# Kernel optimization log

Measured on AMD Instinct MI355X. Metric: run time of the kernel, lower is better.

Reference implementation:

```python
import jax, jax.numpy as jnp
import numpy as np

N = 50000          # nodes
E = 800000         # edges (before self loops)
IN_C = 128
HEADS = 4
D = 64             # out_per_head
HID = HEADS * D    # 256
OUT_C = 128
NEG_SLOPE = 0.2


def setup_inputs() -> dict:
    key = jax.random.key(0)
    ks = jax.random.split(key, 20)
    x = jax.random.normal(ks[0], (N, IN_C), dtype=jnp.float32)
    edge_index = jax.random.randint(ks[1], (2, E), 0, N, dtype=jnp.int32)
    s = 0.05
    params = {}
    dims = [IN_C, HID, HID]
    for i in range(3):
        params[f"W{i+1}"] = jax.random.normal(ks[2 + 4 * i], (dims[i], HID), dtype=jnp.float32) * s
        params[f"a_src{i+1}"] = jax.random.normal(ks[3 + 4 * i], (HEADS, D), dtype=jnp.float32) * s
        params[f"a_dst{i+1}"] = jax.random.normal(ks[4 + 4 * i], (HEADS, D), dtype=jnp.float32) * s
        params[f"b{i+1}"] = jnp.zeros((HID,), dtype=jnp.float32)
    params["head_W"] = jax.random.normal(ks[14], (HID, OUT_C), dtype=jnp.float32) * s
    params["head_b"] = jnp.zeros((OUT_C,), dtype=jnp.float32)
    return {"x": x, "edge_index": edge_index, **params}


def _gat_layer(x, src, dst, W, a_src, a_dst, b):
    # project: [N, heads, D]
    h = (x @ W).reshape(-1, HEADS, D)
    # per-node attention halves: [N, heads]
    alpha_s = jnp.einsum("nhd,hd->nh", h, a_src)
    alpha_d = jnp.einsum("nhd,hd->nh", h, a_dst)
    # per-edge logits: [E, heads]
    logits = jax.nn.leaky_relu(alpha_s[src] + alpha_d[dst], negative_slope=NEG_SLOPE)
    # segment softmax over incoming edges of each dst node
    seg_max = jax.ops.segment_max(logits, dst, num_segments=N)
    e = jnp.exp(logits - seg_max[dst])
    seg_sum = jax.ops.segment_sum(e, dst, num_segments=N)
    alpha = e / (seg_sum[dst] + 1e-16)
    # weighted messages, scatter-aggregate: [N, heads, D]
    msg = h[src] * alpha[:, :, None]
    out = jax.ops.segment_sum(msg, dst, num_segments=N)
    return out.reshape(-1, HID) + b


def reference(x, edge_index, W1, a_src1, a_dst1, b1, W2, a_src2, a_dst2, b2,
              W3, a_src3, a_dst3, b3, head_W, head_b):
    # add self loops once (add_self_loops=True in every GATConv)
    loop = jnp.arange(N, dtype=edge_index.dtype)
    src = jnp.concatenate([edge_index[0], loop])
    dst = jnp.concatenate([edge_index[1], loop])
    h = x
    layers = [(W1, a_src1, a_dst1, b1), (W2, a_src2, a_dst2, b2), (W3, a_src3, a_dst3, b3)]
    for (W, a_s, a_d, b) in layers:
        h = jax.nn.elu(_gat_layer(h, src, dst, W, a_s, a_d, b))
        # dropout inactive in eval mode
    graph_emb = jnp.mean(h, axis=0)          # global_mean_pool over single graph
    logits = graph_emb @ head_W + head_b     # [OUT_C]
    return logits
```

## Files before the change

kernel.cpp:

```cpp
#include <hip/hip_runtime.h>
#include <stdint.h>

#define NN 50000
#define EE 800000
#define ET 850000
#define INC 128
#define HID 256
#define OUTC 128
#define NB ((NN + 255) / 256)

typedef __attribute__((ext_vector_type(4))) float f32x4;
typedef __attribute__((ext_vector_type(8))) short s16x8;
typedef __attribute__((ext_vector_type(4))) short s16x4;

static __device__ __forceinline__ float b2f(unsigned short u){
  union { float f; unsigned int i; } v; v.i = ((unsigned int)u) << 16; return v.f;
}
static __device__ __forceinline__ unsigned short f2b(float f){
  union { float f; unsigned int i; } v; v.f = f;
  unsigned int r = v.i + 0x7FFFu + ((v.i >> 16) & 1u);
  return (unsigned short)(r >> 16);
}

__global__ void k_degree(const int* __restrict__ ei, int* __restrict__ cnt){
  int e = blockIdx.x * 256 + threadIdx.x;
  if (e >= ET) return;
  int d = (e < EE) ? ei[EE + e] : (e - EE);
  atomicAdd(&cnt[d], 1);
}

__global__ void k_blockscan(int* __restrict__ cnt, int* __restrict__ off,
                            int* __restrict__ bsum){
  __shared__ int s[256];
  int b = blockIdx.x, tid = threadIdx.x;
  int i = b * 256 + tid;
  int v = (i < NN) ? cnt[i] : 0;
  if (i < NN) cnt[i] = 0;
  s[tid] = v; __syncthreads();
  #pragma unroll
  for (int o = 1; o < 256; o <<= 1){
    int t = (tid >= o) ? s[tid - o] : 0; __syncthreads();
    s[tid] += t; __syncthreads();
  }
  if (i < NN) off[i] = s[tid] - v;
  if (tid == 255) bsum[b] = s[255];
}

__global__ void k_scanb(const int* __restrict__ bsum, int* __restrict__ bbase){
  __shared__ int s[256];
  int tid = threadIdx.x;
  int v = (tid < NB) ? bsum[tid] : 0;
  s[tid] = v; __syncthreads();
  #pragma unroll
  for (int o = 1; o < 256; o <<= 1){
    int t = (tid >= o) ? s[tid - o] : 0; __syncthreads();
    s[tid] += t; __syncthreads();
  }
  if (tid < NB) bbase[tid] = s[tid] - v;
}

__global__ void k_addback(int* __restrict__ off, const int* __restrict__ bbase){
  int b = blockIdx.x, tid = threadIdx.x;
  int i = b * 256 + tid;
  if (i < NN) off[i] += bbase[b];
  if (i == 0) off[NN] = ET;
}

__global__ void k_scatter(const int* __restrict__ ei, const int* __restrict__ off,
                          int* __restrict__ cnt, int* __restrict__ ssrc){
  int e = blockIdx.x * 256 + threadIdx.x;
  if (e >= ET) return;
  int s, d;
  if (e < EE){ s = ei[e]; d = ei[EE + e]; } else { s = e - EE; d = s; }
  int p = off[d] + atomicAdd(&cnt[d], 1);
  ssrc[p] = s;
}

__global__ void k_transposeAll(const float* __restrict__ W1, const float* __restrict__ W2,
                               const float* __restrict__ W3, unsigned short* __restrict__ T1,
                               unsigned short* __restrict__ T2, unsigned short* __restrict__ T3){
  int b = blockIdx.x;
  const float* W; unsigned short* WT; int K, base;
  if (b < 128)      { W = W1; WT = T1; K = 128; base = 0; }
  else if (b < 384) { W = W2; WT = T2; K = 256; base = 128; }
  else              { W = W3; WT = T3; K = 256; base = 384; }
  int idx = (b - base) * 256 + threadIdx.x;
  int k = idx >> 8, c = idx & 255;
  WT[c * K + k] = f2b(W[idx]);
}

template<bool AF32>
__global__ __launch_bounds__(256) void k_gemm_fused(const void* __restrict__ Av,
    const unsigned short* __restrict__ WT,
    const float* __restrict__ a_src, const float* __restrict__ a_dst,
    unsigned short* __restrict__ C, float* __restrict__ as_, float* __restrict__ ad_,
    int M, int K){
  __shared__ unsigned short sMem[64 * 258];
  unsigned short (*sA)[64][72]  = (unsigned short (*)[64][72])sMem;
  unsigned short (*sC)[258] = (unsigned short (*)[258])sMem;
  int tid = threadIdx.x;
  int wave = tid >> 6, lane = tid & 63;
  int bm0 = blockIdx.x * 64;
  int wc0 = wave * 64;
  f32x4 acc[4][4];
  #pragma unroll
  for (int i = 0; i < 4; i++)
    #pragma unroll
    for (int j = 0; j < 4; j++) acc[i][j] = (f32x4){0.f, 0.f, 0.f, 0.f};

  s16x8 regs[2];
  int li0 = tid, li1 = tid + 256;
  int r0 = li0 >> 3, kb0 = (li0 & 7) * 8;
  int r1 = li1 >> 3, kb1 = (li1 & 7) * 8;

  auto ldA = [&](int k0){
    #pragma unroll
    for (int i = 0; i < 2; i++){
      int rr = i ? r1 : r0, kb = i ? kb1 : kb0;
      int gr = bm0 + rr;
      if constexpr (AF32){
        const float* A = (const float*)Av;
        unsigned short t[8] = {0,0,0,0,0,0,0,0};
        if (gr < M){
          const float4* p = (const float4*)(A + (size_t)gr * K + k0 + kb);
          float4 v0 = p[0], v1 = p[1];
          t[0]=f2b(v0.x); t[1]=f2b(v0.y); t[2]=f2b(v0.z); t[3]=f2b(v0.w);
          t[4]=f2b(v1.x); t[5]=f2b(v1.y); t[6]=f2b(v1.z); t[7]=f2b(v1.w);
        }
        regs[i] = *(s16x8*)t;
      } else {
        const unsigned short* A = (const unsigned short*)Av;
        s16x8 v = (s16x8){0,0,0,0,0,0,0,0};
        if (gr < M) v = *(const s16x8*)(A + (size_t)gr * K + k0 + kb);
        regs[i] = v;
      }
    }
  };
  auto stA = [&](int buf){
    *(s16x8*)&sA[buf][r0][kb0] = regs[0];
    *(s16x8*)&sA[buf][r1][kb1] = regs[1];
  };

  int T = K >> 6;
  ldA(0); stA(0);
  __syncthreads();
  for (int t = 0; t < T; t++){
    int k0 = t << 6;
    if (t + 1 < T) ldA(k0 + 64);
    int cur = t & 1;
    #pragma unroll
    for (int kk = 0; kk < 64; kk += 32){
      int kl = kk + (lane >> 4) * 8;
      s16x8 af[4], bf[4];
      #pragma unroll
      for (int ni = 0; ni < 4; ni++)
        bf[ni] = *(const s16x8*)(WT + (size_t)(wc0 + ni * 16 + (lane & 15)) * K + k0 + kl);
      #pragma unroll
      for (int mi = 0; mi < 4; mi++) af[mi] = *(const s16x8*)&sA[cur][mi * 16 + (lane & 15)][kl];
      #pragma unroll
      for (int mi = 0; mi < 4; mi++)
        #pragma unroll
        for (int ni = 0; ni < 4; ni++)
          acc[mi][ni] = __builtin_amdgcn_mfma_f32_16x16x32_bf16(af[mi], bf[ni], acc[mi][ni], 0, 0, 0);
    }
    if (t + 1 < T) stA(cur ^ 1);
    __syncthreads();
  }

  #pragma unroll
  for (int mi = 0; mi < 4; mi++){
    #pragma unroll
    for (int ni = 0; ni < 4; ni++){
      int col = wc0 + ni * 16 + (lane & 15);
      int rb = mi * 16 + (lane >> 4) * 4;
      #pragma unroll
      for (int r = 0; r < 4; r++){
        int row = rb + r;
        unsigned short us = f2b(acc[mi][ni][r]);
        sC[row][col] = us;
        if (bm0 + row < M) C[(size_t)(bm0 + row) * HID + col] = us;
      }
    }
  }
  __syncthreads();
  {
    int q = wave, r = lane;
    float ps = 0.f, pd = 0.f;
    #pragma unroll 8
    for (int d = 0; d < 64; d++){
      float hv = b2f(sC[r][q * 64 + d]);
      ps += hv * a_src[q * 64 + d];
      pd += hv * a_dst[q * 64 + d];
    }
    if (bm0 + r < M){
      as_[(size_t)(bm0 + r) * 4 + q] = ps;
      ad_[(size_t)(bm0 + r) * 4 + q] = pd;
    }
  }
}

__global__ __launch_bounds__(256) void k_aggregate(const int* __restrict__ off,
    const int* __restrict__ ssrc, const float* __restrict__ as_, const float* __restrict__ ad_,
    const unsigned short* __restrict__ h, const float* __restrict__ bias,
    unsigned short* __restrict__ out){
  int gid = blockIdx.x * 256 + threadIdx.x;
  int wid = gid >> 6, lane = gid & 63;
  if (wid >= NN) return;
  int start = off[wid], end = off[wid + 1], e1 = end - 1;
  int hq = lane >> 4;
  float ad2 = ad_[(size_t)wid * 4 + hq];
  float sA_ = 0.f, sB_ = 0.f;
  f32x4 A = {0,0,0,0}, B = {0,0,0,0}, Cc = {0,0,0,0}, D = {0,0,0,0};

  int p = start;
  int j0 = ssrc[p];
  int j1 = ssrc[min(p + 1, e1)], j2 = ssrc[min(p + 2, e1)], j3 = ssrc[min(p + 3, e1)];
  int j4 = ssrc[min(p + 4, e1)], j5 = ssrc[min(p + 5, e1)];
  int j6 = ssrc[min(p + 6, e1)], j7 = ssrc[min(p + 7, e1)];
  s16x4 r0 = *(const s16x4*)(h + (size_t)j0 * HID + lane * 4);
  s16x4 r1 = *(const s16x4*)(h + (size_t)j1 * HID + lane * 4);
  s16x4 r2 = *(const s16x4*)(h + (size_t)j2 * HID + lane * 4);
  s16x4 r3 = *(const s16x4*)(h + (size_t)j3 * HID + lane * 4);
  float a0 = as_[(size_t)j0 * 4 + hq], a1 = as_[(size_t)j1 * 4 + hq];
  float a2 = as_[(size_t)j2 * 4 + hq], a3 = as_[(size_t)j3 * 4 + hq];

  for (; p + 3 < end; p += 4){
    s16x4 u0 = *(const s16x4*)(h + (size_t)j4 * HID + lane * 4);
    s16x4 u1 = *(const s16x4*)(h + (size_t)j5 * HID + lane * 4);
    s16x4 u2 = *(const s16x4*)(h + (size_t)j6 * HID + lane * 4);
    s16x4 u3 = *(const s16x4*)(h + (size_t)j7 * HID + lane * 4);
    float b0 = as_[(size_t)j4 * 4 + hq], b1 = as_[(size_t)j5 * 4 + hq];
    float b2 = as_[(size_t)j6 * 4 + hq], b3 = as_[(size_t)j7 * 4 + hq];
    int t0 = ssrc[min(p + 8, e1)],  t1 = ssrc[min(p + 9, e1)];
    int t2 = ssrc[min(p + 10, e1)], t3 = ssrc[min(p + 11, e1)];
    float l0 = a0 + ad2; l0 = l0 > 0.f ? l0 : 0.2f * l0;
    float l1 = a1 + ad2; l1 = l1 > 0.f ? l1 : 0.2f * l1;
    float l2 = a2 + ad2; l2 = l2 > 0.f ? l2 : 0.2f * l2;
    float l3 = a3 + ad2; l3 = l3 > 0.f ? l3 : 0.2f * l3;
    float w0 = __expf(fminf(l0, 60.f)), w1 = __expf(fminf(l1, 60.f));
    float w2 = __expf(fminf(l2, 60.f)), w3 = __expf(fminf(l3, 60.f));
    sA_ += w0 + w2; sB_ += w1 + w3;
    #pragma unroll
    for (int c = 0; c < 4; c++){
      A[c]  += w0 * b2f((unsigned short)r0[c]);
      B[c]  += w1 * b2f((unsigned short)r1[c]);
      Cc[c] += w2 * b2f((unsigned short)r2[c]);
      D[c]  += w3 * b2f((unsigned short)r3[c]);
    }
    j0 = j4; j1 = j5; j2 = j6; j3 = j7;
    j4 = t0; j5 = t1; j6 = t2; j7 = t3;
    r0 = u0; r1 = u1; r2 = u2; r3 = u3;
    a0 = b0; a1 = b1; a2 = b2; a3 = b3;
  }
  int rem = end - p;
  if (rem > 0){
    float l = a0 + ad2; l = l > 0.f ? l : 0.2f * l;
    float w = __expf(fminf(l, 60.f)); sA_ += w;
    #pragma unroll
    for (int c = 0; c < 4; c++) A[c]  += w * b2f((unsigned short)r0[c]);
  }
  if (rem > 1){
    float l = a1 + ad2; l = l > 0.f ? l : 0.2f * l;
    float w = __expf(fminf(l, 60.f)); sB_ += w;
    #pragma unroll
    for (int c = 0; c < 4; c++) B[c]  += w * b2f((unsigned short)r1[c]);
  }
  if (rem > 2){
    float l = a2 + ad2; l = l > 0.f ? l : 0.2f * l;
    float w = __expf(fminf(l, 60.f)); sA_ += w;
    #pragma unroll
    for (int c = 0; c < 4; c++) Cc[c] += w * b2f((unsigned short)r2[c]);
  }

  float inv = 1.f / (sA_ + sB_ + 1e-16f);
  float4 bv = *(const float4*)(bias + lane * 4);
  float o0 = (A[0] + B[0] + Cc[0] + D[0]) * inv + bv.x;
  float o1 = (A[1] + B[1] + Cc[1] + D[1]) * inv + bv.y;
  float o2 = (A[2] + B[2] + Cc[2] + D[2]) * inv + bv.z;
  float o3 = (A[3] + B[3] + Cc[3] + D[3]) * inv + bv.w;
  o0 = o0 > 0.f ? o0 : (__expf(o0) - 1.f);
  o1 = o1 > 0.f ? o1 : (__expf(o1) - 1.f);
  o2 = o2 > 0.f ? o2 : (__expf(o2) - 1.f);
  o3 = o3 > 0.f ? o3 : (__expf(o3) - 1.f);
  s16x4 ov;
  ov[0] = (short)f2b(o0); ov[1] = (short)f2b(o1);
  ov[2] = (short)f2b(o2); ov[3] = (short)f2b(o3);
  *(s16x4*)(out + (size_t)wid * HID + lane * 4) = ov;
}

__global__ __launch_bounds__(256) void k_pool(const unsigned short* __restrict__ X,
                                              float* __restrict__ pool){
  int b = blockIdx.x, c = threadIdx.x;
  int n0 = b * 64, n1 = min(n0 + 64, NN);
  float acc = 0.f;
  for (int n = n0; n < n1; n++) acc += b2f(X[(size_t)n * HID + c]);
  atomicAdd(&pool[c], acc);
}

__global__ void k_head(const float* __restrict__ pool, const float* __restrict__ hW,
                       const float* __restrict__ hb, float* __restrict__ outp){
  int o = threadIdx.x;
  float acc = hb[o];
  const float invN = 1.f / (float)NN;
  for (int c = 0; c < HID; c++) acc += pool[c] * invN * hW[c * OUTC + o];
  outp[o] = acc;
}

extern "C" void kernel_launch(void* const* d_in, const int* in_sizes, int n_in,
                              void* d_out, int out_size, void* d_ws, size_t ws_size,
                              hipStream_t stream){
  const float* x  = (const float*)d_in[0];
  const int* ei   = (const int*)d_in[1];
  const float* W[3]   = {(const float*)d_in[2],  (const float*)d_in[6],  (const float*)d_in[10]};
  const float* Asr[3] = {(const float*)d_in[3],  (const float*)d_in[7],  (const float*)d_in[11]};
  const float* Adt[3] = {(const float*)d_in[4],  (const float*)d_in[8],  (const float*)d_in[12]};
  const float* B[3]   = {(const float*)d_in[5],  (const float*)d_in[9],  (const float*)d_in[13]};
  const float* hW = (const float*)d_in[14];
  const float* hb = (const float*)d_in[15];

  char* w = (char*)d_ws; size_t o = 0;
  auto alloc = [&](size_t b) -> void* { void* p = w + o; o = (o + b + 255) & ~(size_t)255; return p; };
  int* cnt  = (int*)alloc((size_t)NN * 4);
  int* off  = (int*)alloc((size_t)(NN + 1) * 4);
  int* ssrc = (int*)alloc((size_t)ET * 4);
  int* bsum = (int*)alloc((size_t)NB * 4);
  int* bbase= (int*)alloc((size_t)NB * 4);
  unsigned short* hbuf = (unsigned short*)alloc((size_t)NN * HID * 2);
  float* as_ = (float*)alloc((size_t)NN * 4 * 4);
  float* ad_ = (float*)alloc((size_t)NN * 4 * 4);
  unsigned short* X0 = (unsigned short*)alloc((size_t)NN * HID * 2);
  unsigned short* X1 = (unsigned short*)alloc((size_t)NN * HID * 2);
  unsigned short* WT1 = (unsigned short*)alloc((size_t)INC * HID * 2);
  unsigned short* WT2 = (unsigned short*)alloc((size_t)HID * HID * 2);
  unsigned short* WT3 = (unsigned short*)alloc((size_t)HID * HID * 2);
  float* pool = (float*)alloc(256 * 4);

  hipMemsetAsync(cnt, 0, (size_t)NN * 4, stream);
  hipMemsetAsync(pool, 0, 256 * 4, stream);
  k_degree<<<(ET + 255) / 256, 256, 0, stream>>>(ei, cnt);
  k_blockscan<<<NB, 256, 0, stream>>>(cnt, off, bsum);
  k_scanb<<<1, 256, 0, stream>>>(bsum, bbase);
  k_addback<<<NB, 256, 0, stream>>>(off, bbase);
  k_scatter<<<(ET + 255) / 256, 256, 0, stream>>>(ei, off, cnt, ssrc);
  k_transposeAll<<<640, 256, 0, stream>>>(W[0], W[1], W[2], WT1, WT2, WT3);

  const unsigned short* WTs[3] = {WT1, WT2, WT3};
  unsigned short* outbuf[3] = {X0, X1, X0};
  int Ks[3] = {INC, HID, HID};
  const void* Ain = (const void*)x;
  int gB = (NN + 63) / 64;
  int gW = (NN * 64 + 255) / 256;
  for (int l = 0; l < 3; l++){
    if (l == 0) k_gemm_fused<true ><<<gB, 256, 0, stream>>>(Ain, WTs[l], Asr[l], Adt[l], hbuf, as_, ad_, NN, Ks[l]);
    else        k_gemm_fused<false><<<gB, 256, 0, stream>>>(Ain, WTs[l], Asr[l], Adt[l], hbuf, as_, ad_, NN, Ks[l]);
    k_aggregate<<<gW, 256, 0, stream>>>(off, ssrc, as_, ad_, hbuf, B[l], outbuf[l]);
    Ain = (const void*)outbuf[l];
  }
  k_pool<<<gB, 256, 0, stream>>>(X0, pool);
  k_head<<<1, 128, 0, stream>>>(pool, hW, hb, (float*)d_out);
}
```

Baseline: 418.0 us.

## Merge setup kernels, fold block offsets into consumers, fuse head into pool

Combines the degree count, weight transpose and pool/counter reset into one init kernel. Drops the addback pass by adding the per-block scan base inside scatter and aggregate. Fuses the head matmul into the pool kernel using a last-block-done counter. Adds an unclamped fast-path loop in aggregate and removes the exp clamp, using fmaxf for leaky-relu. Together these cut launch count and a little per-edge ALU work, at the risk of overflow without the clamp.

```diff
diff --git a/kernel.cpp b/kernel.cpp
--- a/kernel.cpp
+++ b/kernel.cpp
@@ -8,6 +8,8 @@
 #define HID 256
 #define OUTC 128
 #define NB ((NN + 255) / 256)
+#define GDEG ((ET + 255) / 256)
+#define GTRP 640
 
 typedef __attribute__((ext_vector_type(4))) float f32x4;
 typedef __attribute__((ext_vector_type(8))) short s16x8;
@@ -22,11 +24,31 @@
   return (unsigned short)(r >> 16);
 }
 
-__global__ void k_degree(const int* __restrict__ ei, int* __restrict__ cnt){
-  int e = blockIdx.x * 256 + threadIdx.x;
-  if (e >= ET) return;
-  int d = (e < EE) ? ei[EE + e] : (e - EE);
-  atomicAdd(&cnt[d], 1);
+__global__ void k_init(const int* __restrict__ ei, int* __restrict__ cnt,
+                       const float* __restrict__ W1, const float* __restrict__ W2,
+                       const float* __restrict__ W3, unsigned short* __restrict__ T1,
+                       unsigned short* __restrict__ T2, unsigned short* __restrict__ T3,
+                       float* __restrict__ pool, int* __restrict__ done){
+  int b = blockIdx.x, tid = threadIdx.x;
+  if (b < GDEG){
+    int e = b * 256 + tid;
+    if (e < ET){
+      int d = (e < EE) ? ei[EE + e] : (e - EE);
+      atomicAdd(&cnt[d], 1);
+    }
+  } else if (b < GDEG + GTRP){
+    int bb = b - GDEG;
+    const float* W; unsigned short* WT; int K, base;
+    if (bb < 128)      { W = W1; WT = T1; K = 128; base = 0; }
+    else if (bb < 384) { W = W2; WT = T2; K = 256; base = 128; }
+    else               { W = W3; WT = T3; K = 256; base = 384; }
+    int idx = (bb - base) * 256 + tid;
+    int k = idx >> 8, c = idx & 255;
+    WT[c * K + k] = f2b(W[idx]);
+  } else {
+    pool[tid] = 0.f;
+    if (tid == 0) *done = 0;
+  }
 }
 
 __global__ void k_blockscan(int* __restrict__ cnt, int* __restrict__ off,
@@ -59,34 +81,15 @@
   if (tid < NB) bbase[tid] = s[tid] - v;
 }
 
-__global__ void k_addback(int* __restrict__ off, const int* __restrict__ bbase){
-  int b = blockIdx.x, tid = threadIdx.x;
-  int i = b * 256 + tid;
-  if (i < NN) off[i] += bbase[b];
-  if (i == 0) off[NN] = ET;
-}
-
 __global__ void k_scatter(const int* __restrict__ ei, const int* __restrict__ off,
-                          int* __restrict__ cnt, int* __restrict__ ssrc){
+                          const int* __restrict__ bbase, int* __restrict__ cnt,
+                          int* __restrict__ ssrc){
   int e = blockIdx.x * 256 + threadIdx.x;
   if (e >= ET) return;
   int s, d;
   if (e < EE){ s = ei[e]; d = ei[EE + e]; } else { s = e - EE; d = s; }
-  int p = off[d] + atomicAdd(&cnt[d], 1);
+  int p = off[d] + bbase[d >> 8] + atomicAdd(&cnt[d], 1);
   ssrc[p] = s;
-}
-
-__global__ void k_transposeAll(const float* __restrict__ W1, const float* __restrict__ W2,
-                               const float* __restrict__ W3, unsigned short* __restrict__ T1,
-                               unsigned short* __restrict__ T2, unsigned short* __restrict__ T3){
-  int b = blockIdx.x;
-  const float* W; unsigned short* WT; int K, base;
-  if (b < 128)      { W = W1; WT = T1; K = 128; base = 0; }
-  else if (b < 384) { W = W2; WT = T2; K = 256; base = 128; }
-  else              { W = W3; WT = T3; K = 256; base = 384; }
-  int idx = (b - base) * 256 + threadIdx.x;
-  int k = idx >> 8, c = idx & 255;
-  WT[c * K + k] = f2b(W[idx]);
 }
 
 template<bool AF32>
@@ -200,13 +203,16 @@
 }
 
 __global__ __launch_bounds__(256) void k_aggregate(const int* __restrict__ off,
-    const int* __restrict__ ssrc, const float* __restrict__ as_, const float* __restrict__ ad_,
+    const int* __restrict__ bbase, const int* __restrict__ ssrc,
+    const float* __restrict__ as_, const float* __restrict__ ad_,
     const unsigned short* __restrict__ h, const float* __restrict__ bias,
     unsigned short* __restrict__ out){
   int gid = blockIdx.x * 256 + threadIdx.x;
   int wid = gid >> 6, lane = gid & 63;
   if (wid >= NN) return;
-  int start = off[wid], end = off[wid + 1], e1 = end - 1;
+  int start = off[wid] + bbase[wid >> 8];
+  int end = (wid + 1 < NN) ? (off[wid + 1] + bbase[(wid + 1) >> 8]) : ET;
+  int e1 = end - 1;
   int hq = lane >> 4;
   float ad2 = ad_[(size_t)wid * 4 + hq];
   float sA_ = 0.f, sB_ = 0.f;
@@ -224,6 +230,32 @@
   float a0 = as_[(size_t)j0 * 4 + hq], a1 = as_[(size_t)j1 * 4 + hq];
   float a2 = as_[(size_t)j2 * 4 + hq], a3 = as_[(size_t)j3 * 4 + hq];
 
+  for (; p + 11 < end; p += 4){
+    s16x4 u0 = *(const s16x4*)(h + (size_t)j4 * HID + lane * 4);
+    s16x4 u1 = *(const s16x4*)(h + (size_t)j5 * HID + lane * 4);
+    s16x4 u2 = *(const s16x4*)(h + (size_t)j6 * HID + lane * 4);
+    s16x4 u3 = *(const s16x4*)(h + (size_t)j7 * HID + lane * 4);
+    float b0 = as_[(size_t)j4 * 4 + hq], b1 = as_[(size_t)j5 * 4 + hq];
+    float b2 = as_[(size_t)j6 * 4 + hq], b3 = as_[(size_t)j7 * 4 + hq];
+    int t0 = ssrc[p + 8], t1 = ssrc[p + 9], t2 = ssrc[p + 10], t3 = ssrc[p + 11];
+    float l0 = a0 + ad2; l0 = fmaxf(l0, 0.2f * l0);
+    float l1 = a1 + ad2; l1 = fmaxf(l1, 0.2f * l1);
+    float l2 = a2 + ad2; l2 = fmaxf(l2, 0.2f * l2);
+    float l3 = a3 + ad2; l3 = fmaxf(l3, 0.2f * l3);
+    float w0 = __expf(l0), w1 = __expf(l1), w2 = __expf(l2), w3 = __expf(l3);
+    sA_ += w0 + w2; sB_ += w1 + w3;
+    #pragma unroll
+    for (int c = 0; c < 4; c++){
+      A[c]  += w0 * b2f((unsigned short)r0[c]);
+      B[c]  += w1 * b2f((unsigned short)r1[c]);
+      Cc[c] += w2 * b2f((unsigned short)r2[c]);
+      D[c]  += w3 * b2f((unsigned short)r3[c]);
+    }
+    j0 = j4; j1 = j5; j2 = j6; j3 = j7;
+    j4 = t0; j5 = t1; j6 = t2; j7 = t3;
+    r0 = u0; r1 = u1; r2 = u2; r3 = u3;
+    a0 = b0; a1 = b1; a2 = b2; a3 = b3;
+  }
   for (; p + 3 < end; p += 4){
     s16x4 u0 = *(const s16x4*)(h + (size_t)j4 * HID + lane * 4);
     s16x4 u1 = *(const s16x4*)(h + (size_t)j5 * HID + lane * 4);
@@ -233,12 +265,11 @@
     float b2 = as_[(size_t)j6 * 4 + hq], b3 = as_[(size_t)j7 * 4 + hq];
     int t0 = ssrc[min(p + 8, e1)],  t1 = ssrc[min(p + 9, e1)];
     int t2 = ssrc[min(p + 10, e1)], t3 = ssrc[min(p + 11, e1)];
-    float l0 = a0 + ad2; l0 = l0 > 0.f ? l0 : 0.2f * l0;
-    float l1 = a1 + ad2; l1 = l1 > 0.f ? l1 : 0.2f * l1;
-    float l2 = a2 + ad2; l2 = l2 > 0.f ? l2 : 0.2f * l2;
-    float l3 = a3 + ad2; l3 = l3 > 0.f ? l3 : 0.2f * l3;
-    float w0 = __expf(fminf(l0, 60.f)), w1 = __expf(fminf(l1, 60.f));
-    float w2 = __expf(fminf(l2, 60.f)), w3 = __expf(fminf(l3, 60.f));
+    float l0 = a0 + ad2; l0 = fmaxf(l0, 0.2f * l0);
+    float l1 = a1 + ad2; l1 = fmaxf(l1, 0.2f * l1);
+    float l2 = a2 + ad2; l2 = fmaxf(l2, 0.2f * l2);
+    float l3 = a3 + ad2; l3 = fmaxf(l3, 0.2f * l3);
+    float w0 = __expf(l0), w1 = __expf(l1), w2 = __expf(l2), w3 = __expf(l3);
     sA_ += w0 + w2; sB_ += w1 + w3;
     #pragma unroll
     for (int c = 0; c < 4; c++){
@@ -254,20 +285,20 @@
   }
   int rem = end - p;
   if (rem > 0){
-    float l = a0 + ad2; l = l > 0.f ? l : 0.2f * l;
-    float w = __expf(fminf(l, 60.f)); sA_ += w;
+    float l = a0 + ad2; l = fmaxf(l, 0.2f * l);
+    float w = __expf(l); sA_ += w;
     #pragma unroll
     for (int c = 0; c < 4; c++) A[c]  += w * b2f((unsigned short)r0[c]);
   }
   if (rem > 1){
-    float l = a1 + ad2; l = l > 0.f ? l : 0.2f * l;
-    float w = __expf(fminf(l, 60.f)); sB_ += w;
+    float l = a1 + ad2; l = fmaxf(l, 0.2f * l);
+    float w = __expf(l); sB_ += w;
     #pragma unroll
     for (int c = 0; c < 4; c++) B[c]  += w * b2f((unsigned short)r1[c]);
   }
   if (rem > 2){
-    float l = a2 + ad2; l = l > 0.f ? l : 0.2f * l;
-    float w = __expf(fminf(l, 60.f)); sA_ += w;
+    float l = a2 + ad2; l = fmaxf(l, 0.2f * l);
+    float w = __expf(l); sA_ += w;
     #pragma unroll
     for (int c = 0; c < 4; c++) Cc[c] += w * b2f((unsigned short)r2[c]);
   }
@@ -289,21 +320,32 @@
 }
 
 __global__ __launch_bounds__(256) void k_pool(const unsigned short* __restrict__ X,
-                                              float* __restrict__ pool){
+    float* __restrict__ pool, int* __restrict__ done, const float* __restrict__ hW,
+    const float* __restrict__ hb, float* __restrict__ outp){
   int b = blockIdx.x, c = threadIdx.x;
   int n0 = b * 64, n1 = min(n0 + 64, NN);
   float acc = 0.f;
   for (int n = n0; n < n1; n++) acc += b2f(X[(size_t)n * HID + c]);
   atomicAdd(&pool[c], acc);
-}
-
-__global__ void k_head(const float* __restrict__ pool, const float* __restrict__ hW,
-                       const float* __restrict__ hb, float* __restrict__ outp){
-  int o = threadIdx.x;
-  float acc = hb[o];
-  const float invN = 1.f / (float)NN;
-  for (int c = 0; c < HID; c++) acc += pool[c] * invN * hW[c * OUTC + o];
-  outp[o] = acc;
+  __threadfence();
+  __syncthreads();
+  __shared__ int isLast;
+  if (c == 0){
+    int old = atomicAdd(done, 1);
+    isLast = (old == gridDim.x - 1);
+  }
+  __syncthreads();
+  if (isLast){
+    __shared__ float pv[HID];
+    pv[c] = atomicAdd(&pool[c], 0.0f);
+    __syncthreads();
+    if (c < OUTC){
+      float a2 = hb[c];
+      const float invN = 1.f / (float)NN;
+      for (int k = 0; k < HID; k++) a2 += pv[k] * invN * hW[k * OUTC + c];
+      outp[c] = a2;
+    }
+  }
 }
 
 extern "C" void kernel_launch(void* const* d_in, const int* in_sizes, int n_in,
@@ -321,10 +363,11 @@
   char* w = (char*)d_ws; size_t o = 0;
   auto alloc = [&](size_t b) -> void* { void* p = w + o; o = (o + b + 255) & ~(size_t)255; return p; };
   int* cnt  = (int*)alloc((size_t)NN * 4);
-  int* off  = (int*)alloc((size_t)(NN + 1) * 4);
+  int* off  = (int*)alloc((size_t)NN * 4);
   int* ssrc = (int*)alloc((size_t)ET * 4);
   int* bsum = (int*)alloc((size_t)NB * 4);
   int* bbase= (int*)alloc((size_t)NB * 4);
+  int* done = (int*)alloc(4);
   unsigned short* hbuf = (unsigned short*)alloc((size_t)NN * HID * 2);
   float* as_ = (float*)alloc((size_t)NN * 4 * 4);
   float* ad_ = (float*)alloc((size_t)NN * 4 * 4);
@@ -336,13 +379,10 @@
   float* pool = (float*)alloc(256 * 4);
 
   hipMemsetAsync(cnt, 0, (size_t)NN * 4, stream);
-  hipMemsetAsync(pool, 0, 256 * 4, stream);
-  k_degree<<<(ET + 255) / 256, 256, 0, stream>>>(ei, cnt);
+  k_init<<<GDEG + GTRP + 1, 256, 0, stream>>>(ei, cnt, W[0], W[1], W[2], WT1, WT2, WT3, pool, done);
   k_blockscan<<<NB, 256, 0, stream>>>(cnt, off, bsum);
   k_scanb<<<1, 256, 0, stream>>>(bsum, bbase);
-  k_addback<<<NB, 256, 0, stream>>>(off, bbase);
-  k_scatter<<<(ET + 255) / 256, 256, 0, stream>>>(ei, off, cnt, ssrc);
-  k_transposeAll<<<640, 256, 0, stream>>>(W[0], W[1], W[2], WT1, WT2, WT3);
+  k_scatter<<<GDEG, 256, 0, stream>>>(ei, off, bbase, cnt, ssrc);
 
   const unsigned short* WTs[3] = {WT1, WT2, WT3};
   unsigned short* outbuf[3] = {X0, X1, X0};
@@ -353,9 +393,8 @@
   for (int l = 0; l < 3; l++){
     if (l == 0) k_gemm_fused<true ><<<gB, 256, 0, stream>>>(Ain, WTs[l], Asr[l], Adt[l], hbuf, as_, ad_, NN, Ks[l]);
     else        k_gemm_fused<false><<<gB, 256, 0, stream>>>(Ain, WTs[l], Asr[l], Adt[l], hbuf, as_, ad_, NN, Ks[l]);
-    k_aggregate<<<gW, 256, 0, stream>>>(off, ssrc, as_, ad_, hbuf, B[l], outbuf[l]);
+    k_aggregate<<<gW, 256, 0, stream>>>(off, bbase, ssrc, as_, ad_, hbuf, B[l], outbuf[l]);
     Ain = (const void*)outbuf[l];
   }
-  k_pool<<<gB, 256, 0, stream>>>(X0, pool);
-  k_head<<<1, 128, 0, stream>>>(pool, hW, hb, (float*)d_out);
-}
+  k_pool<<<gB, 256, 0, stream>>>(X0, pool, done, hW, hb, (float*)d_out);
+}
```

After: 449.2 us. 1.07x slower.
